# Kernel optimization log

Hardware: AMD Instinct MI355X
Metric: run time of the kernel (lower is better)

The kernel has to match this reference:

```python
import jax, jax.numpy as jnp
import numpy as np

B, N, K, D, H, T = 32, 4096, 8, 256, 4, 3
DH = D // H
SCALE = DH ** -0.5
EPS = 1e-8
HID = 256


def layernorm(x, w, b, eps=1e-5):
    m = jnp.mean(x, axis=-1, keepdims=True)
    v = jnp.var(x, axis=-1, keepdims=True)
    return (x - m) * jax.lax.rsqrt(v + eps) * w + b


def setup_inputs() -> dict:
    key = jax.random.key(0)
    ks = jax.random.split(key, 20)
    p = 0.02
    inp = {
        "x": jax.random.normal(ks[0], (B, N, D), jnp.float32),
        "noise": jax.random.normal(ks[1], (B, K, D), jnp.float32),
        "mu": jax.random.normal(ks[2], (1, 1, D), jnp.float32),
        "log_sigma": jax.random.normal(ks[3], (1, 1, D), jnp.float32) * p,
        "norm_in_w": jnp.ones((D,), jnp.float32), "norm_in_b": jnp.zeros((D,), jnp.float32),
        "norm_slot_w": jnp.ones((D,), jnp.float32), "norm_slot_b": jnp.zeros((D,), jnp.float32),
        "norm_mlp_w": jnp.ones((D,), jnp.float32), "norm_mlp_b": jnp.zeros((D,), jnp.float32),
        "Wq": jax.random.normal(ks[4], (D, D), jnp.float32) * p,
        "Wk": jax.random.normal(ks[5], (D, D), jnp.float32) * p,
        "Wv": jax.random.normal(ks[6], (D, D), jnp.float32) * p,
        "Wo": jax.random.normal(ks[7], (D, D), jnp.float32) * p,
        "gru_Wih": jax.random.normal(ks[8], (3 * D, D), jnp.float32) * p,
        "gru_Whh": jax.random.normal(ks[9], (3 * D, D), jnp.float32) * p,
        "gru_bih": jnp.zeros((3 * D,), jnp.float32),
        "gru_bhh": jnp.zeros((3 * D,), jnp.float32),
        "mlp_W1": jax.random.normal(ks[10], (HID, D), jnp.float32) * p,
        "mlp_b1": jnp.zeros((HID,), jnp.float32),
        "mlp_W2": jax.random.normal(ks[11], (D, HID), jnp.float32) * p,
        "mlp_b2": jnp.zeros((D,), jnp.float32),
    }
    return inp


def _split(t):
    # [b, n, D] -> [b, H, n, d_h]
    b, n, _ = t.shape
    return t.reshape(b, n, H, DH).transpose(0, 2, 1, 3)


def _merge(t):
    # [b, H, n, d_h] -> [b, n, D]
    b, h, n, d = t.shape
    return t.transpose(0, 2, 1, 3).reshape(b, n, h * d)


def _step(slots, k_feat, v_feat, p):
    b, k, d = slots.shape
    q = _split(layernorm(slots, p["norm_slot_w"], p["norm_slot_b"]) @ p["Wq"].T)
    dots = jnp.einsum("bhkd,bhnd->bhkn", q, k_feat) * SCALE
    attn = jax.nn.softmax(dots, axis=2)              # softmax over slot (query) axis
    attn = attn / (jnp.sum(attn, axis=-1, keepdims=True) + EPS)  # renorm over keys
    upd = _merge(jnp.einsum("bhkn,bhnd->bhkd", attn, v_feat)) @ p["Wo"].T
    # GRUCell(update, slots)
    gi = upd @ p["gru_Wih"].T + p["gru_bih"]
    gh = slots @ p["gru_Whh"].T + p["gru_bhh"]
    i_r, i_z, i_n = jnp.split(gi, 3, axis=-1)
    h_r, h_z, h_n = jnp.split(gh, 3, axis=-1)
    r = jax.nn.sigmoid(i_r + h_r)
    z = jax.nn.sigmoid(i_z + h_z)
    n = jnp.tanh(i_n + r * h_n)
    slots = (1.0 - z) * n + z * slots
    h1 = jax.nn.relu(layernorm(slots, p["norm_mlp_w"], p["norm_mlp_b"]) @ p["mlp_W1"].T + p["mlp_b1"])
    return slots + h1 @ p["mlp_W2"].T + p["mlp_b2"]


def reference(x, noise, mu, log_sigma, norm_in_w, norm_in_b, norm_slot_w, norm_slot_b,
              norm_mlp_w, norm_mlp_b, Wq, Wk, Wv, Wo, gru_Wih, gru_Whh, gru_bih, gru_bhh,
              mlp_W1, mlp_b1, mlp_W2, mlp_b2):
    p = dict(norm_slot_w=norm_slot_w, norm_slot_b=norm_slot_b, norm_mlp_w=norm_mlp_w,
             norm_mlp_b=norm_mlp_b, Wq=Wq, Wo=Wo, gru_Wih=gru_Wih, gru_Whh=gru_Whh,
             gru_bih=gru_bih, gru_bhh=gru_bhh, mlp_W1=mlp_W1, mlp_b1=mlp_b1,
             mlp_W2=mlp_W2, mlp_b2=mlp_b2)
    slots = mu + jnp.exp(log_sigma) * noise          # [B, K, D]
    xn = layernorm(x, norm_in_w, norm_in_b)
    k_feat = _split(xn @ Wk.T)                       # [B, H, N, d_h]
    v_feat = _split(xn @ Wv.T)
    for _ in range(T):
        slots = _step(slots, k_feat, v_feat, p)
    return slots
```

## Files before the change

### kernel.cpp

```cpp
#include <hip/hip_runtime.h>
#include <stdint.h>

typedef unsigned short ushort_t;
typedef __attribute__((ext_vector_type(8))) short bfrag;
typedef __attribute__((ext_vector_type(4))) float ffrag;

#define B_  32
#define K_  8
#define N_  4096
#define D_  256
#define H_  4
#define DH_ 64

__device__ __forceinline__ ushort_t f2bf(float f) {
  unsigned int u = __builtin_bit_cast(unsigned int, f);
  u += 0x7FFFu + ((u >> 16) & 1u);
  return (ushort_t)(u >> 16);
}

__global__ __launch_bounds__(256) void k_stats(const float* __restrict__ x,
                                               float2* __restrict__ stats) {
  int row = blockIdx.x * 4 + (threadIdx.x >> 6);
  int lane = threadIdx.x & 63;
  const float4* xr = (const float4*)(x + (size_t)row * 256);
  float4 v = xr[lane];
  float s = v.x + v.y + v.z + v.w;
  float q = v.x*v.x + v.y*v.y + v.z*v.z + v.w*v.w;
  #pragma unroll
  for (int off = 32; off >= 1; off >>= 1) { s += __shfl_xor(s, off); q += __shfl_xor(q, off); }
  if (lane == 0) {
    float m = s * (1.f/256.f);
    float var = q * (1.f/256.f) - m * m;
    stats[row] = make_float2(m, rsqrtf(var + 1e-5f));
  }
}

__global__ __launch_bounds__(256) void k_prep_wkv(const float* __restrict__ Wk, const float* __restrict__ Wv,
                                                  const float* __restrict__ lnw, const float* __restrict__ lnb,
                                                  ushort_t* __restrict__ wkv,
                                                  float* __restrict__ c1, float* __restrict__ c2) {
  int n = blockIdx.x;
  int i = threadIdx.x;
  float wv = (n < 256) ? Wk[n*256 + i] : Wv[(n-256)*256 + i];
  float wp = lnw[i] * wv;
  wkv[n*256 + i] = f2bf(wp);
  float p1 = wp, p2 = lnb[i] * wv;
  #pragma unroll
  for (int off = 32; off >= 1; off >>= 1) { p1 += __shfl_xor(p1, off); p2 += __shfl_xor(p2, off); }
  __shared__ float r1[4], r2[4];
  int w = threadIdx.x >> 6;
  if ((threadIdx.x & 63) == 0) { r1[w] = p1; r2[w] = p2; }
  __syncthreads();
  if (threadIdx.x == 0) { c1[n] = r1[0]+r1[1]+r1[2]+r1[3]; c2[n] = r2[0]+r2[1]+r2[2]+r2[3]; }
}

__global__ __launch_bounds__(256) void k_prep_wf(const float* __restrict__ Wih, const float* __restrict__ Wo,
                                                 float* __restrict__ Wf) {
  int j = blockIdx.x;
  int i = threadIdx.x;
  __shared__ float row[256];
  row[i] = Wih[j*256 + i];
  __syncthreads();
  float acc = 0.f;
  #pragma unroll 8
  for (int t = 0; t < 256; ++t) acc += row[t] * Wo[t*256 + i];
  Wf[j*256 + i] = acc;
}

__device__ __forceinline__ void row_ln_256(float (*S)[256], float (*L)[256],
                                           const float* __restrict__ w, const float* __restrict__ b, int t) {
  int k = t >> 5, ln = t & 31;
  float s = 0.f, q = 0.f;
  #pragma unroll
  for (int j = 0; j < 8; ++j) { float v = S[k][ln + j*32]; s += v; q += v*v; }
  #pragma unroll
  for (int off = 16; off >= 1; off >>= 1) { s += __shfl_xor(s, off); q += __shfl_xor(q, off); }
  float m = s * (1.f/256.f);
  float rstd = rsqrtf(q * (1.f/256.f) - m*m + 1e-5f);
  #pragma unroll
  for (int j = 0; j < 8; ++j) {
    int c = ln + j*32;
    L[k][c] = (S[k][c] - m) * rstd * w[c] + b[c];
  }
}

__device__ __forceinline__ void qproj(float (*L)[256], const float* __restrict__ Wq,
                                      ushort_t* __restrict__ qbuf, int b, int t) {
  int c = t;
  const float4* Wrow = (const float4*)(Wq + (size_t)c * 256);
  float acc[8];
  #pragma unroll
  for (int k = 0; k < 8; ++k) acc[k] = 0.f;
  for (int i = 0; i < 64; ++i) {
    float4 wv = Wrow[i];
    #pragma unroll
    for (int k = 0; k < 8; ++k) {
      float4 xv = *((const float4*)&L[k][0] + i);
      acc[k] = fmaf(xv.x, wv.x, fmaf(xv.y, wv.y, fmaf(xv.z, wv.z, fmaf(xv.w, wv.w, acc[k]))));
    }
  }
  int h = c >> 6, dh = c & 63;
  ushort_t* dst = qbuf + ((size_t)(b*4 + h) * 16) * 64 + dh;
  #pragma unroll
  for (int k = 0; k < 8; ++k) dst[k*64] = f2bf(acc[k] * 0.125f);
  #pragma unroll
  for (int k = 8; k < 16; ++k) dst[k*64] = 0;
}

__global__ __launch_bounds__(256) void k_init(const float* __restrict__ noise, const float* __restrict__ mu,
                                              const float* __restrict__ lsig, float* __restrict__ slots,
                                              const float* __restrict__ nsw, const float* __restrict__ nsb,
                                              const float* __restrict__ Wq, ushort_t* __restrict__ qbuf) {
  int b = blockIdx.x, t = threadIdx.x;
  __shared__ float S[8][256];
  __shared__ float L[8][256];
  float e = __expf(lsig[t]);
  float m = mu[t];
  #pragma unroll
  for (int k = 0; k < 8; ++k) {
    float v = m + e * noise[((size_t)(b*8+k))*256 + t];
    S[k][t] = v;
    slots[((size_t)(b*8+k))*256 + t] = v;
  }
  __syncthreads();
  row_ln_256(S, L, nsw, nsb, t);
  __syncthreads();
  qproj(L, Wq, qbuf, b, t);
}

__global__ __launch_bounds__(256, 2) void k_gemm(const float* __restrict__ x, const float2* __restrict__ stats,
                                                 const ushort_t* __restrict__ wkv,
                                                 const float* __restrict__ c1, const float* __restrict__ c2,
                                                 ushort_t* __restrict__ kf, ushort_t* __restrict__ vfT) {
  int mb = blockIdx.x, cb = blockIdx.y;
  int t = threadIdx.x;
  int w = t >> 6, l = t & 63;
  __shared__ uint4 ldsv[4096];
  char* lds = (char*)ldsv;
  const int m0 = mb * 128;
  const int col0 = cb * 128;

  int r0 = t >> 1, half = t & 1;
  float4 xa[8];
  uint4 wb[4];

  auto loadA = [&](int s) {
    const float4* src = (const float4*)(x + (size_t)(m0 + r0) * 256 + s*64 + half*32);
    #pragma unroll
    for (int i = 0; i < 8; ++i) xa[i] = src[i];
  };
  auto loadB = [&](int s) {
    const uint4* src = (const uint4*)(wkv + (size_t)(col0 + r0) * 256 + s*64 + half*32);
    #pragma unroll
    for (int i = 0; i < 4; ++i) wb[i] = src[i];
  };
  auto writeA = [&](char* Ab) {
    #pragma unroll
    for (int i = 0; i < 4; ++i) {
      float4 a = xa[2*i], b2 = xa[2*i+1];
      union { ushort_t us[8]; uint4 v; } u;
      u.us[0]=f2bf(a.x);  u.us[1]=f2bf(a.y);  u.us[2]=f2bf(a.z);  u.us[3]=f2bf(a.w);
      u.us[4]=f2bf(b2.x); u.us[5]=f2bf(b2.y); u.us[6]=f2bf(b2.z); u.us[7]=f2bf(b2.w);
      int byte = (r0*128 + half*64 + i*16) ^ ((r0 & 7) << 4);
      *(uint4*)(Ab + byte) = u.v;
    }
  };
  auto writeB = [&](char* Bb) {
    #pragma unroll
    for (int i = 0; i < 4; ++i) {
      int byte = (r0*128 + half*64 + i*16) ^ ((r0 & 7) << 4);
      *(uint4*)(Bb + byte) = wb[i];
    }
  };

  ffrag acc[4][4];
  #pragma unroll
  for (int i = 0; i < 4; ++i)
    #pragma unroll
    for (int j = 0; j < 4; ++j) acc[i][j] = (ffrag){0.f,0.f,0.f,0.f};

  int wm = w & 1, wn = w >> 1;
  int lrow = l & 15, lk = (l >> 4) * 8;

  loadA(0); loadB(0);
  writeA(lds + 0); writeB(lds + 32768);
  __syncthreads();

  for (int s = 0; s < 4; ++s) {
    char* Ac = lds + ((s & 1) ? 16384 : 0);
    char* Bc = lds + 32768 + ((s & 1) ? 16384 : 0);
    if (s < 3) { loadA(s+1); loadB(s+1); }
    #pragma unroll
    for (int kk = 0; kk < 2; ++kk) {
      bfrag af[4], bf[4];
      #pragma unroll
      for (int i = 0; i < 4; ++i) {
        int row = wm*64 + i*16 + lrow;
        int byte = (row*128 + (kk*32 + lk)*2) ^ ((row & 7) << 4);
        af[i] = *(const bfrag*)(Ac + byte);
      }
      #pragma unroll
      for (int j = 0; j < 4; ++j) {
        int row = wn*64 + j*16 + lrow;
        int byte = (row*128 + (kk*32 + lk)*2) ^ ((row & 7) << 4);
        bf[j] = *(const bfrag*)(Bc + byte);
      }
      #pragma unroll
      for (int i = 0; i < 4; ++i)
        #pragma unroll
        for (int j = 0; j < 4; ++j)
          acc[i][j] = __builtin_amdgcn_mfma_f32_16x16x32_bf16(af[i], bf[j], acc[i][j], 0, 0, 0);
    }
    if (s < 3) {
      char* An = lds + ((s & 1) ? 0 : 16384);
      char* Bn = lds + 32768 + ((s & 1) ? 0 : 16384);
      writeA(An); writeB(Bn);
    }
    __syncthreads();
  }

  int g = l >> 4, nl = l & 15;
  int b = m0 >> 12;
  int nx0 = m0 & 4095;
  if (cb < 2) {
    char* Ct = lds;
    #pragma unroll
    for (int i = 0; i < 4; ++i) {
      #pragma unroll
      for (int j = 0; j < 4; ++j) {
        int coll = wn*64 + j*16 + nl;
        float cc1 = c1[col0 + coll], cc2 = c2[col0 + coll];
        #pragma unroll
        for (int r = 0; r < 4; ++r) {
          int ml = wm*64 + i*16 + g*4 + r;
          float2 st = stats[m0 + ml];
          float val = st.y * (acc[i][j][r] - st.x * cc1) + cc2;
          *(ushort_t*)(Ct + (ml*136 + coll)*2) = f2bf(val);
        }
      }
    }
    __syncthreads();
    int m = t >> 1, hh = t & 1;
    int h = cb*2 + hh;
    ushort_t* dst = kf + ((size_t)((b*4 + h)*4096 + nx0 + m)) * 64;
    const char* srcr = Ct + m*272 + hh*128;
    #pragma unroll
    for (int jj = 0; jj < 8; ++jj)
      ((uint4*)dst)[jj] = *(const uint4*)(srcr + jj*16);
  } else {
    char* Ct = lds;
    #pragma unroll
    for (int i = 0; i < 4; ++i) {
      int mlbase = wm*64 + i*16 + g*4;
      #pragma unroll
      for (int j = 0; j < 4; ++j) {
        int coll = wn*64 + j*16 + nl;
        float cc1 = c1[col0 + coll], cc2 = c2[col0 + coll];
        ushort_t us[4];
        #pragma unroll
        for (int r = 0; r < 4; ++r) {
          float2 st = stats[m0 + mlbase + r];
          us[r] = f2bf(st.y * (acc[i][j][r] - st.x * cc1) + cc2);
        }
        uint2 pk = make_uint2((unsigned)us[0] | ((unsigned)us[1] << 16),
                              (unsigned)us[2] | ((unsigned)us[3] << 16));
        *(uint2*)(Ct + coll*272 + mlbase*2) = pk;
      }
    }
    __syncthreads();
    int colt = t >> 1, hh = t & 1;
    int h = (cb - 2)*2 + (colt >> 6);
    int dh = colt & 63;
    ushort_t* dst = vfT + ((size_t)((b*4 + h)*64 + dh)) * 4096 + nx0 + hh*64;
    const char* srcr = Ct + colt*272 + hh*128;
    #pragma unroll
    for (int jj = 0; jj < 8; ++jj)
      ((uint4*)dst)[jj] = *(const uint4*)(srcr + jj*16);
  }
}

__global__ __launch_bounds__(256, 2) void k_attn(const ushort_t* __restrict__ q, const ushort_t* __restrict__ kf,
                                                 const ushort_t* __restrict__ vfT,
                                                 float* __restrict__ updp, float* __restrict__ asump) {
  int split = blockIdx.x;
  int bh = blockIdx.y;
  int n0 = split * 256;
  int t = threadIdx.x, w = t >> 6, l = t & 63;
  __shared__ uint4 ldsv[4736];
  char* lds = (char*)ldsv;
  char* Kt = lds;
  char* Vt = lds + 32768;
  char* Pl = lds + 65536;
  char* Ql = lds + 73728;

  {
    const uint4* src = (const uint4*)(kf + ((size_t)bh*4096 + n0 + t) * 64);
    #pragma unroll
    for (int i = 0; i < 8; ++i) {
      int byte = (t*128 + i*16) ^ ((t & 7) << 4);
      *(uint4*)(Kt + byte) = src[i];
    }
  }
  {
    int d = t >> 2, seg = t & 3;
    const uint4* src = (const uint4*)(vfT + ((size_t)bh*64 + d) * 4096 + n0 + seg*64);
    #pragma unroll
    for (int i = 0; i < 4; ++i) {
      int byte = (d*512 + seg*128 + i*16) ^ ((d & 7) << 4);
      *(uint4*)(Vt + byte) = src[i];
    }
  }
  if (t < 128) {
    int k = t >> 3, seg = t & 7;
    uint4 v = *(const uint4*)(q + ((size_t)bh*16 + k) * 64 + seg*8);
    int byte = (k*128 + seg*16) ^ ((k & 7) << 4);
    *(uint4*)(Ql + byte) = v;
  }
  *(uint4*)(Pl + 4096 + t*16) = make_uint4(0,0,0,0);
  __syncthreads();

  int g = l >> 4, nl = l & 15, lk = g * 8;

  ffrag dacc[4];
  #pragma unroll
  for (int nt = 0; nt < 4; ++nt) {
    dacc[nt] = (ffrag){0.f,0.f,0.f,0.f};
    #pragma unroll
    for (int kk = 0; kk < 2; ++kk) {
      int qbyte = (nl*128 + (kk*32 + lk)*2) ^ ((nl & 7) << 4);
      bfrag af = *(const bfrag*)(Ql + qbyte);
      int row = w*64 + nt*16 + nl;
      int kbyte = (row*128 + (kk*32 + lk)*2) ^ ((row & 7) << 4);
      bfrag bf = *(const bfrag*)(Kt + kbyte);
      dacc[nt] = __builtin_amdgcn_mfma_f32_16x16x32_bf16(af, bf, dacc[nt], 0, 0, 0);
    }
  }

  float asr0 = 0.f, asr1 = 0.f, asr2 = 0.f, asr3 = 0.f;
  #pragma unroll
  for (int nt = 0; nt < 4; ++nt) {
    float d0 = dacc[nt][0], d1 = dacc[nt][1], d2 = dacc[nt][2], d3 = dacc[nt][3];
    float mx = fmaxf(fmaxf(d0, d1), fmaxf(d2, d3));
    mx = fmaxf(mx, __shfl_xor(mx, 16));
    float p0 = __expf(d0 - mx), p1 = __expf(d1 - mx), p2 = __expf(d2 - mx), p3 = __expf(d3 - mx);
    float sden = p0 + p1 + p2 + p3;
    sden += __shfl_xor(sden, 16);
    float inv = 1.f / sden;
    p0 *= inv; p1 *= inv; p2 *= inv; p3 *= inv;
    if (g < 2) {
      asr0 += p0; asr1 += p1; asr2 += p2; asr3 += p3;
      int n = w*64 + nt*16 + nl;
      int k0 = g*4;
      *(ushort_t*)(Pl + (((k0+0)*512 + n*2) ^ (((k0+0)&7) << 4))) = f2bf(p0);
      *(ushort_t*)(Pl + (((k0+1)*512 + n*2) ^ (((k0+1)&7) << 4))) = f2bf(p1);
      *(ushort_t*)(Pl + (((k0+2)*512 + n*2) ^ (((k0+2)&7) << 4))) = f2bf(p2);
      *(ushort_t*)(Pl + (((k0+3)*512 + n*2) ^ (((k0+3)&7) << 4))) = f2bf(p3);
    }
  }
  #pragma unroll
  for (int off = 8; off >= 1; off >>= 1) {
    asr0 += __shfl_xor(asr0, off); asr1 += __shfl_xor(asr1, off);
    asr2 += __shfl_xor(asr2, off); asr3 += __shfl_xor(asr3, off);
  }
  if (g < 2 && nl == 0) {
    float* dst = asump + (((size_t)bh*16 + split)*4 + w)*8 + g*4;
    dst[0] = asr0; dst[1] = asr1; dst[2] = asr2; dst[3] = asr3;
  }
  __syncthreads();

  ffrag pacc = (ffrag){0.f,0.f,0.f,0.f};
  #pragma unroll
  for (int ni = 0; ni < 8; ++ni) {
    int nn = ni * 32;
    int pbyte = (nl*512 + (nn + lk)*2) ^ ((nl & 7) << 4);
    bfrag af = *(const bfrag*)(Pl + pbyte);
    int d = w*16 + nl;
    int vbyte = (d*512 + (nn + lk)*2) ^ ((d & 7) << 4);
    bfrag bf = *(const bfrag*)(Vt + vbyte);
    pacc = __builtin_amdgcn_mfma_f32_16x16x32_bf16(af, bf, pacc, 0, 0, 0);
  }
  if (g < 2) {
    float* dst = updp + (((size_t)bh*16 + split)*8 + g*4)*64 + w*16 + nl;
    #pragma unroll
    for (int r = 0; r < 4; ++r) dst[r*64] = pacc[r];
  }
}

__global__ __launch_bounds__(256) void k_fin(const float* __restrict__ updp, const float* __restrict__ asump,
                                             float* __restrict__ upd) {
  int bh = blockIdx.x, t = threadIdx.x;
  __shared__ float asum[8];
  if (t < 8) {
    float a = 0.f;
    for (int s = 0; s < 64; ++s) a += asump[((size_t)bh*64 + s)*8 + t];
    asum[t] = a + 1e-8f;
  }
  __syncthreads();
  int b = bh >> 2, h = bh & 3;
  #pragma unroll
  for (int o = t; o < 512; o += 256) {
    int k = o >> 6, d = o & 63;
    float u = 0.f;
    for (int s = 0; s < 16; ++s) u += updp[(((size_t)bh*16 + s)*8 + k)*64 + d];
    upd[((size_t)(b*8 + k))*256 + h*64 + d] = u / asum[k];
  }
}

__global__ __launch_bounds__(256) void k_u1(const float* __restrict__ upd, const float* __restrict__ slots,
                                            const float* __restrict__ Wf, const float* __restrict__ Whh,
                                            const float* __restrict__ bih, const float* __restrict__ bhh,
                                            float* __restrict__ gi, float* __restrict__ gh) {
  int cb = blockIdx.x, b = blockIdx.y, t = threadIdx.x;
  int c = cb * 256 + t;
  bool isGi = (c < 768);
  __shared__ float X[8][256];
  const float* src = isGi ? upd : slots;
  #pragma unroll
  for (int k = 0; k < 8; ++k) X[k][t] = src[((size_t)(b*8+k))*256 + t];
  __syncthreads();
  int cc = isGi ? c : (c - 768);
  const float* Wrow = (isGi ? Wf : Whh) + (size_t)cc * 256;
  float bias = isGi ? bih[cc] : bhh[cc];
  float acc[8];
  #pragma unroll
  for (int k = 0; k < 8; ++k) acc[k] = bias;
  for (int i = 0; i < 64; ++i) {
    float4 wv = ((const float4*)Wrow)[i];
    #pragma unroll
    for (int k = 0; k < 8; ++k) {
      float4 xv = *((const float4*)&X[k][0] + i);
      acc[k] = fmaf(xv.x, wv.x, fmaf(xv.y, wv.y, fmaf(xv.z, wv.z, fmaf(xv.w, wv.w, acc[k]))));
    }
  }
  float* dst = isGi ? gi : gh;
  #pragma unroll
  for (int k = 0; k < 8; ++k) dst[((size_t)(b*8+k))*768 + cc] = acc[k];
}

__global__ __launch_bounds__(256) void k_u2(const float* __restrict__ gi, const float* __restrict__ gh,
                                            const float* __restrict__ slots_in, float* __restrict__ slots_out,
                                            const float* __restrict__ nmw, const float* __restrict__ nmb,
                                            const float* __restrict__ W1, const float* __restrict__ b1,
                                            const float* __restrict__ W2, const float* __restrict__ b2,
                                            const float* __restrict__ nsw, const float* __restrict__ nsb,
                                            const float* __restrict__ Wq, ushort_t* __restrict__ qbuf, int do_q) {
  int b = blockIdx.x, t = threadIdx.x;
  __shared__ float S[8][256];
  __shared__ float L[8][256];
  __shared__ float H1[8][256];
  #pragma unroll
  for (int k = 0; k < 8; ++k) {
    size_t gb = ((size_t)(b*8+k))*768;
    float ir = gi[gb + t],       hr = gh[gb + t];
    float iz = gi[gb + 256 + t], hz = gh[gb + 256 + t];
    float in_ = gi[gb + 512 + t], hn = gh[gb + 512 + t];
    float r = 1.f / (1.f + __expf(-(ir + hr)));
    float z = 1.f / (1.f + __expf(-(iz + hz)));
    float a = in_ + r * hn;
    float e2 = __expf(-2.f * fabsf(a));
    float nn = (1.f - e2) / (1.f + e2);
    nn = copysignf(nn, a);
    S[k][t] = (1.f - z) * nn + z * slots_in[((size_t)(b*8+k))*256 + t];
  }
  __syncthreads();
  row_ln_256(S, L, nmw, nmb, t);
  __syncthreads();
  {
    const float4* Wrow = (const float4*)(W1 + (size_t)t * 256);
    float bb = b1[t];
    float acc[8];
    #pragma unroll
    for (int k = 0; k < 8; ++k) acc[k] = bb;
    for (int i = 0; i < 64; ++i) {
      float4 wv = Wrow[i];
      #pragma unroll
      for (int k = 0; k < 8; ++k) {
        float4 xv = *((const float4*)&L[k][0] + i);
        acc[k] = fmaf(xv.x, wv.x, fmaf(xv.y, wv.y, fmaf(xv.z, wv.z, fmaf(xv.w, wv.w, acc[k]))));
      }
    }
    #pragma unroll
    for (int k = 0; k < 8; ++k) H1[k][t] = fmaxf(acc[k], 0.f);
  }
  __syncthreads();
  {
    const float4* Wrow = (const float4*)(W2 + (size_t)t * 256);
    float bb = b2[t];
    float acc[8];
    #pragma unroll
    for (int k = 0; k < 8; ++k) acc[k] = bb;
    for (int i = 0; i < 64; ++i) {
      float4 wv = Wrow[i];
      #pragma unroll
      for (int k = 0; k < 8; ++k) {
        float4 xv = *((const float4*)&H1[k][0] + i);
        acc[k] = fmaf(xv.x, wv.x, fmaf(xv.y, wv.y, fmaf(xv.z, wv.z, fmaf(xv.w, wv.w, acc[k]))));
      }
    }
    #pragma unroll
    for (int k = 0; k < 8; ++k) {
      float o = S[k][t] + acc[k];
      slots_out[((size_t)(b*8+k))*256 + t] = o;
      S[k][t] = o;
    }
  }
  __syncthreads();
  if (do_q) {
    row_ln_256(S, L, nsw, nsb, t);
    __syncthreads();
    qproj(L, Wq, qbuf, b, t);
  }
}

extern "C" void kernel_launch(void* const* d_in, const int* in_sizes, int n_in,
                              void* d_out, int out_size, void* d_ws, size_t ws_size,
                              hipStream_t stream) {
  (void)in_sizes; (void)n_in; (void)out_size; (void)ws_size;
  const float* x     = (const float*)d_in[0];
  const float* noise = (const float*)d_in[1];
  const float* mu    = (const float*)d_in[2];
  const float* lsig  = (const float*)d_in[3];
  const float* ninw  = (const float*)d_in[4];
  const float* ninb  = (const float*)d_in[5];
  const float* nsw   = (const float*)d_in[6];
  const float* nsb   = (const float*)d_in[7];
  const float* nmw   = (const float*)d_in[8];
  const float* nmb   = (const float*)d_in[9];
  const float* Wq    = (const float*)d_in[10];
  const float* Wk    = (const float*)d_in[11];
  const float* Wv    = (const float*)d_in[12];
  const float* Wo    = (const float*)d_in[13];
  const float* Wih   = (const float*)d_in[14];
  const float* Whh   = (const float*)d_in[15];
  const float* bih   = (const float*)d_in[16];
  const float* bhh   = (const float*)d_in[17];
  const float* W1    = (const float*)d_in[18];
  const float* b1    = (const float*)d_in[19];
  const float* W2    = (const float*)d_in[20];
  const float* b2    = (const float*)d_in[21];

  char* ws = (char*)d_ws;
  float2*   stats = (float2*)  (ws + 0);
  ushort_t* wkv   = (ushort_t*)(ws + 1048576);
  float*    c1    = (float*)   (ws + 1310720);
  float*    c2    = (float*)   (ws + 1312768);
  float*    Wf    = (float*)   (ws + 1314816);
  float*    slots = (float*)   (ws + 2101248);
  ushort_t* qbuf  = (ushort_t*)(ws + 2363392);
  float*    upd   = (float*)   (ws + 2625536);
  float*    gi    = (float*)   (ws + 2887680);
  float*    gh    = (float*)   (ws + 3674112);
  float*    asump = (float*)   (ws + 4460544);
  float*    updp  = (float*)   (ws + 4722688);
  ushort_t* kf    = (ushort_t*)(ws + 8916992);
  ushort_t* vfT   = (ushort_t*)(ws + 76025856);

  k_stats   <<<32768, 256, 0, stream>>>(x, stats);
  k_prep_wkv<<<512,   256, 0, stream>>>(Wk, Wv, ninw, ninb, wkv, c1, c2);
  k_prep_wf <<<768,   256, 0, stream>>>(Wih, Wo, Wf);
  k_init    <<<32,    256, 0, stream>>>(noise, mu, lsig, slots, nsw, nsb, Wq, qbuf);
  k_gemm    <<<dim3(1024, 4), 256, 0, stream>>>(x, stats, wkv, c1, c2, kf, vfT);

  float* outp = (float*)d_out;
  for (int it = 0; it < 3; ++it) {
    k_attn<<<dim3(16, 128), 256, 0, stream>>>(qbuf, kf, vfT, updp, asump);
    k_fin <<<128, 256, 0, stream>>>(updp, asump, upd);
    k_u1  <<<dim3(6, 32), 256, 0, stream>>>(upd, slots, Wf, Whh, bih, bhh, gi, gh);
    k_u2  <<<32, 256, 0, stream>>>(gi, gh, slots, (it == 2) ? outp : slots,
                                   nmw, nmb, W1, b1, W2, b2, nsw, nsb, Wq, qbuf, (it < 2) ? 1 : 0);
  }
}
```

Baseline: 644.1 us.

## Fuse layernorm stats into K/V GEMM, shrink LDS, read K/V directly in attention

The separate row-statistics kernel is removed. Mean and rstd are now accumulated in the GEMM's A-tile load path and shared through LDS, which avoids one extra full pass over x. The GEMM uses a smaller K-step with half the LDS, raises occupancy to 4 blocks per unit, and remaps block IDs into groups of 8. Its epilogue is split into two halves. The attention kernel drops its K/V LDS staging and reads MFMA fragments straight from global memory, and k_u2 is split across two blocks per batch; each of these trades memory locality or redundant weight reads for more parallelism.

```diff
diff --git a/kernel.cpp b/kernel.cpp
--- a/kernel.cpp
+++ b/kernel.cpp
@@ -16,23 +16,6 @@
   unsigned int u = __builtin_bit_cast(unsigned int, f);
   u += 0x7FFFu + ((u >> 16) & 1u);
   return (ushort_t)(u >> 16);
-}
-
-__global__ __launch_bounds__(256) void k_stats(const float* __restrict__ x,
-                                               float2* __restrict__ stats) {
-  int row = blockIdx.x * 4 + (threadIdx.x >> 6);
-  int lane = threadIdx.x & 63;
-  const float4* xr = (const float4*)(x + (size_t)row * 256);
-  float4 v = xr[lane];
-  float s = v.x + v.y + v.z + v.w;
-  float q = v.x*v.x + v.y*v.y + v.z*v.z + v.w*v.w;
-  #pragma unroll
-  for (int off = 32; off >= 1; off >>= 1) { s += __shfl_xor(s, off); q += __shfl_xor(q, off); }
-  if (lane == 0) {
-    float m = s * (1.f/256.f);
-    float var = q * (1.f/256.f) - m * m;
-    stats[row] = make_float2(m, rsqrtf(var + 1e-5f));
-  }
 }
 
 __global__ __launch_bounds__(256) void k_prep_wkv(const float* __restrict__ Wk, const float* __restrict__ Wv,
@@ -107,6 +90,46 @@
   for (int k = 8; k < 16; ++k) dst[k*64] = 0;
 }
 
+__device__ __forceinline__ void row_ln_4x(float (*S)[256], float (*L)[256],
+                                          const float* __restrict__ w, const float* __restrict__ b, int t) {
+  int k = t >> 6, ln = t & 63;
+  float s = 0.f, q = 0.f;
+  #pragma unroll
+  for (int j = 0; j < 4; ++j) { float v = S[k][ln + j*64]; s += v; q += v*v; }
+  #pragma unroll
+  for (int off = 32; off >= 1; off >>= 1) { s += __shfl_xor(s, off); q += __shfl_xor(q, off); }
+  float m = s * (1.f/256.f);
+  float rstd = rsqrtf(q * (1.f/256.f) - m*m + 1e-5f);
+  #pragma unroll
+  for (int j = 0; j < 4; ++j) {
+    int c = ln + j*64;
+    L[k][c] = (S[k][c] - m) * rstd * w[c] + b[c];
+  }
+}
+
+__device__ __forceinline__ void qproj4(float (*L)[256], const float* __restrict__ Wq,
+                                       ushort_t* __restrict__ qbuf, int b, int ks0, int t) {
+  int c = t;
+  const float4* Wrow = (const float4*)(Wq + (size_t)c * 256);
+  float acc[4];
+  #pragma unroll
+  for (int k = 0; k < 4; ++k) acc[k] = 0.f;
+  for (int i = 0; i < 64; ++i) {
+    float4 wv = Wrow[i];
+    #pragma unroll
+    for (int k = 0; k < 4; ++k) {
+      float4 xv = *((const float4*)&L[k][0] + i);
+      acc[k] = fmaf(xv.x, wv.x, fmaf(xv.y, wv.y, fmaf(xv.z, wv.z, fmaf(xv.w, wv.w, acc[k]))));
+    }
+  }
+  int h = c >> 6, dh = c & 63;
+  ushort_t* dst = qbuf + ((size_t)(b*4 + h) * 16) * 64 + dh;
+  #pragma unroll
+  for (int k = 0; k < 4; ++k) dst[(ks0 + k)*64] = f2bf(acc[k] * 0.125f);
+  #pragma unroll
+  for (int k = 0; k < 4; ++k) dst[(8 + ks0 + k)*64] = 0;
+}
+
 __global__ __launch_bounds__(256) void k_init(const float* __restrict__ noise, const float* __restrict__ mu,
                                               const float* __restrict__ lsig, float* __restrict__ slots,
                                               const float* __restrict__ nsw, const float* __restrict__ nsb,
@@ -128,210 +151,205 @@
   qproj(L, Wq, qbuf, b, t);
 }
 
-__global__ __launch_bounds__(256, 2) void k_gemm(const float* __restrict__ x, const float2* __restrict__ stats,
+__global__ __launch_bounds__(256, 4) void k_gemm(const float* __restrict__ x,
                                                  const ushort_t* __restrict__ wkv,
                                                  const float* __restrict__ c1, const float* __restrict__ c2,
                                                  ushort_t* __restrict__ kf, ushort_t* __restrict__ vfT) {
-  int mb = blockIdx.x, cb = blockIdx.y;
-  int t = threadIdx.x;
-  int w = t >> 6, l = t & 63;
-  __shared__ uint4 ldsv[4096];
+  int bid = blockIdx.x;
+  int wg = (bid & 7) * 512 + (bid >> 3);
+  int mb = wg >> 2, cb = wg & 3;
+  int t = threadIdx.x, w = t >> 6, l = t & 63;
+  __shared__ uint4 ldsv[2048];
   char* lds = (char*)ldsv;
-  const int m0 = mb * 128;
-  const int col0 = cb * 128;
-
+  const int m0 = mb * 128, col0 = cb * 128;
   int r0 = t >> 1, half = t & 1;
-  float4 xa[8];
-  uint4 wb[4];
+
+  float4 xa[4];
+  uint4 wb[2];
+  float ssum = 0.f, sqsum = 0.f;
+  int swzW = ((r0 >> 1) & 3) << 4;
 
   auto loadA = [&](int s) {
-    const float4* src = (const float4*)(x + (size_t)(m0 + r0) * 256 + s*64 + half*32);
-    #pragma unroll
-    for (int i = 0; i < 8; ++i) xa[i] = src[i];
+    const float4* src = (const float4*)(x + (size_t)(m0 + r0) * 256 + s*32 + half*16);
+    #pragma unroll
+    for (int i = 0; i < 4; ++i) xa[i] = src[i];
   };
   auto loadB = [&](int s) {
-    const uint4* src = (const uint4*)(wkv + (size_t)(col0 + r0) * 256 + s*64 + half*32);
-    #pragma unroll
-    for (int i = 0; i < 4; ++i) wb[i] = src[i];
+    const uint4* src = (const uint4*)(wkv + (size_t)(col0 + r0) * 256 + s*32 + half*16);
+    wb[0] = src[0]; wb[1] = src[1];
   };
   auto writeA = [&](char* Ab) {
     #pragma unroll
-    for (int i = 0; i < 4; ++i) {
+    for (int i = 0; i < 2; ++i) {
       float4 a = xa[2*i], b2 = xa[2*i+1];
+      ssum  += a.x + a.y + a.z + a.w + b2.x + b2.y + b2.z + b2.w;
+      sqsum += a.x*a.x + a.y*a.y + a.z*a.z + a.w*a.w
+             + b2.x*b2.x + b2.y*b2.y + b2.z*b2.z + b2.w*b2.w;
       union { ushort_t us[8]; uint4 v; } u;
       u.us[0]=f2bf(a.x);  u.us[1]=f2bf(a.y);  u.us[2]=f2bf(a.z);  u.us[3]=f2bf(a.w);
       u.us[4]=f2bf(b2.x); u.us[5]=f2bf(b2.y); u.us[6]=f2bf(b2.z); u.us[7]=f2bf(b2.w);
-      int byte = (r0*128 + half*64 + i*16) ^ ((r0 & 7) << 4);
-      *(uint4*)(Ab + byte) = u.v;
+      *(uint4*)(Ab + r0*64 + ((half*32 + i*16) ^ swzW)) = u.v;
     }
   };
   auto writeB = [&](char* Bb) {
     #pragma unroll
+    for (int i = 0; i < 2; ++i)
+      *(uint4*)(Bb + r0*64 + ((half*32 + i*16) ^ swzW)) = wb[i];
+  };
+
+  ffrag acc[4][4];
+  #pragma unroll
+  for (int i = 0; i < 4; ++i)
+    #pragma unroll
+    for (int j = 0; j < 4; ++j) acc[i][j] = (ffrag){0.f,0.f,0.f,0.f};
+
+  int wm = w & 1, wn = w >> 1;
+  int lrow = l & 15, lkb = ((l >> 4) * 8) * 2;
+
+  loadA(0); loadB(0);
+  writeA(lds); writeB(lds + 16384);
+  __syncthreads();
+
+  for (int s = 0; s < 8; ++s) {
+    char* Ac = lds + ((s & 1) << 13);
+    char* Bc = lds + 16384 + ((s & 1) << 13);
+    if (s < 7) { loadA(s+1); loadB(s+1); }
+    bfrag bfr[4];
+    #pragma unroll
+    for (int j = 0; j < 4; ++j) {
+      int row = wn*64 + j*16 + lrow;
+      bfr[j] = *(const bfrag*)(Bc + row*64 + (lkb ^ (((row >> 1) & 3) << 4)));
+    }
+    #pragma unroll
     for (int i = 0; i < 4; ++i) {
-      int byte = (r0*128 + half*64 + i*16) ^ ((r0 & 7) << 4);
-      *(uint4*)(Bb + byte) = wb[i];
-    }
-  };
-
-  ffrag acc[4][4];
-  #pragma unroll
-  for (int i = 0; i < 4; ++i)
-    #pragma unroll
-    for (int j = 0; j < 4; ++j) acc[i][j] = (ffrag){0.f,0.f,0.f,0.f};
-
-  int wm = w & 1, wn = w >> 1;
-  int lrow = l & 15, lk = (l >> 4) * 8;
-
-  loadA(0); loadB(0);
-  writeA(lds + 0); writeB(lds + 32768);
-  __syncthreads();
-
-  for (int s = 0; s < 4; ++s) {
-    char* Ac = lds + ((s & 1) ? 16384 : 0);
-    char* Bc = lds + 32768 + ((s & 1) ? 16384 : 0);
-    if (s < 3) { loadA(s+1); loadB(s+1); }
-    #pragma unroll
-    for (int kk = 0; kk < 2; ++kk) {
-      bfrag af[4], bf[4];
+      int row = wm*64 + i*16 + lrow;
+      bfrag afr = *(const bfrag*)(Ac + row*64 + (lkb ^ (((row >> 1) & 3) << 4)));
       #pragma unroll
-      for (int i = 0; i < 4; ++i) {
-        int row = wm*64 + i*16 + lrow;
-        int byte = (row*128 + (kk*32 + lk)*2) ^ ((row & 7) << 4);
-        af[i] = *(const bfrag*)(Ac + byte);
-      }
-      #pragma unroll
-      for (int j = 0; j < 4; ++j) {
-        int row = wn*64 + j*16 + lrow;
-        int byte = (row*128 + (kk*32 + lk)*2) ^ ((row & 7) << 4);
-        bf[j] = *(const bfrag*)(Bc + byte);
-      }
-      #pragma unroll
-      for (int i = 0; i < 4; ++i)
+      for (int j = 0; j < 4; ++j)
+        acc[i][j] = __builtin_amdgcn_mfma_f32_16x16x32_bf16(afr, bfr[j], acc[i][j], 0, 0, 0);
+    }
+    if (s < 7) {
+      char* An = lds + (((s+1) & 1) << 13);
+      char* Bn = lds + 16384 + (((s+1) & 1) << 13);
+      writeA(An); writeB(Bn);
+    }
+    __syncthreads();
+  }
+
+  float s2 = ssum  + __shfl_xor(ssum, 1);
+  float q2 = sqsum + __shfl_xor(sqsum, 1);
+  float* statm = (float*)(lds + 28672);
+  float* statr = (float*)(lds + 29184);
+  if (half == 0) {
+    float mm = s2 * (1.f/256.f);
+    statm[r0] = mm;
+    statr[r0] = rsqrtf(q2 * (1.f/256.f) - mm*mm + 1e-5f);
+  }
+  __syncthreads();
+
+  int g = l >> 4, nl = l & 15;
+  int b = m0 >> 12, nx0 = m0 & 4095;
+  if (cb < 2) {
+    for (int p = 0; p < 2; ++p) {
+      if (wm == p) {
         #pragma unroll
-        for (int j = 0; j < 4; ++j)
-          acc[i][j] = __builtin_amdgcn_mfma_f32_16x16x32_bf16(af[i], bf[j], acc[i][j], 0, 0, 0);
-    }
-    if (s < 3) {
-      char* An = lds + ((s & 1) ? 0 : 16384);
-      char* Bn = lds + 32768 + ((s & 1) ? 0 : 16384);
-      writeA(An); writeB(Bn);
-    }
-    __syncthreads();
-  }
-
-  int g = l >> 4, nl = l & 15;
-  int b = m0 >> 12;
-  int nx0 = m0 & 4095;
-  if (cb < 2) {
-    char* Ct = lds;
-    #pragma unroll
-    for (int i = 0; i < 4; ++i) {
-      #pragma unroll
-      for (int j = 0; j < 4; ++j) {
-        int coll = wn*64 + j*16 + nl;
-        float cc1 = c1[col0 + coll], cc2 = c2[col0 + coll];
-        #pragma unroll
-        for (int r = 0; r < 4; ++r) {
-          int ml = wm*64 + i*16 + g*4 + r;
-          float2 st = stats[m0 + ml];
-          float val = st.y * (acc[i][j][r] - st.x * cc1) + cc2;
-          *(ushort_t*)(Ct + (ml*136 + coll)*2) = f2bf(val);
+        for (int i = 0; i < 4; ++i) {
+          #pragma unroll
+          for (int j = 0; j < 4; ++j) {
+            int coll = wn*64 + j*16 + nl;
+            float cc1 = c1[col0 + coll], cc2 = c2[col0 + coll];
+            #pragma unroll
+            for (int r = 0; r < 4; ++r) {
+              int ml = i*16 + g*4 + r;
+              int mlg = p*64 + ml;
+              float val = statr[mlg] * (acc[i][j][r] - statm[mlg] * cc1) + cc2;
+              *(ushort_t*)(lds + (ml*136 + coll)*2) = f2bf(val);
+            }
+          }
         }
       }
-    }
-    __syncthreads();
-    int m = t >> 1, hh = t & 1;
-    int h = cb*2 + hh;
-    ushort_t* dst = kf + ((size_t)((b*4 + h)*4096 + nx0 + m)) * 64;
-    const char* srcr = Ct + m*272 + hh*128;
-    #pragma unroll
-    for (int jj = 0; jj < 8; ++jj)
-      ((uint4*)dst)[jj] = *(const uint4*)(srcr + jj*16);
+      __syncthreads();
+      {
+        int mloc = t >> 2, hh = (t >> 1) & 1, qq = t & 1;
+        int h = cb*2 + hh;
+        ushort_t* dst = kf + ((size_t)((b*4 + h)*4096 + nx0 + p*64 + mloc)) * 64 + qq*32;
+        const char* srcr = lds + mloc*272 + hh*128 + qq*64;
+        #pragma unroll
+        for (int jj = 0; jj < 4; ++jj)
+          ((uint4*)dst)[jj] = *(const uint4*)(srcr + jj*16);
+      }
+      __syncthreads();
+    }
   } else {
-    char* Ct = lds;
-    #pragma unroll
-    for (int i = 0; i < 4; ++i) {
-      int mlbase = wm*64 + i*16 + g*4;
-      #pragma unroll
-      for (int j = 0; j < 4; ++j) {
-        int coll = wn*64 + j*16 + nl;
-        float cc1 = c1[col0 + coll], cc2 = c2[col0 + coll];
-        ushort_t us[4];
+    for (int p = 0; p < 2; ++p) {
+      if (wn == p) {
         #pragma unroll
-        for (int r = 0; r < 4; ++r) {
-          float2 st = stats[m0 + mlbase + r];
-          us[r] = f2bf(st.y * (acc[i][j][r] - st.x * cc1) + cc2);
+        for (int i = 0; i < 4; ++i) {
+          int mlb = wm*64 + i*16 + g*4;
+          #pragma unroll
+          for (int j = 0; j < 4; ++j) {
+            int coll = j*16 + nl;
+            int collg = p*64 + coll;
+            float cc1 = c1[col0 + collg], cc2 = c2[col0 + collg];
+            ushort_t us[4];
+            #pragma unroll
+            for (int r = 0; r < 4; ++r)
+              us[r] = f2bf(statr[mlb+r] * (acc[i][j][r] - statm[mlb+r] * cc1) + cc2);
+            *(uint2*)(lds + coll*272 + mlb*2) =
+              make_uint2((unsigned)us[0] | ((unsigned)us[1] << 16),
+                         (unsigned)us[2] | ((unsigned)us[3] << 16));
+          }
         }
-        uint2 pk = make_uint2((unsigned)us[0] | ((unsigned)us[1] << 16),
-                              (unsigned)us[2] | ((unsigned)us[3] << 16));
-        *(uint2*)(Ct + coll*272 + mlbase*2) = pk;
       }
-    }
-    __syncthreads();
-    int colt = t >> 1, hh = t & 1;
-    int h = (cb - 2)*2 + (colt >> 6);
-    int dh = colt & 63;
-    ushort_t* dst = vfT + ((size_t)((b*4 + h)*64 + dh)) * 4096 + nx0 + hh*64;
-    const char* srcr = Ct + colt*272 + hh*128;
-    #pragma unroll
-    for (int jj = 0; jj < 8; ++jj)
-      ((uint4*)dst)[jj] = *(const uint4*)(srcr + jj*16);
-  }
-}
-
-__global__ __launch_bounds__(256, 2) void k_attn(const ushort_t* __restrict__ q, const ushort_t* __restrict__ kf,
+      __syncthreads();
+      {
+        int cl = t >> 2, seg = t & 3;
+        int collg = p*64 + cl;
+        int h = (cb - 2)*2 + (collg >> 6);
+        int dh = collg & 63;
+        ushort_t* dst = vfT + ((size_t)((b*4 + h)*64 + dh)) * 4096 + nx0 + seg*32;
+        const char* srcr = lds + cl*272 + seg*64;
+        #pragma unroll
+        for (int jj = 0; jj < 4; ++jj)
+          ((uint4*)dst)[jj] = *(const uint4*)(srcr + jj*16);
+      }
+      __syncthreads();
+    }
+  }
+}
+
+__global__ __launch_bounds__(256, 4) void k_attn(const ushort_t* __restrict__ q, const ushort_t* __restrict__ kf,
                                                  const ushort_t* __restrict__ vfT,
                                                  float* __restrict__ updp, float* __restrict__ asump) {
   int split = blockIdx.x;
   int bh = blockIdx.y;
   int n0 = split * 256;
   int t = threadIdx.x, w = t >> 6, l = t & 63;
-  __shared__ uint4 ldsv[4736];
+  __shared__ uint4 ldsv[640];
   char* lds = (char*)ldsv;
-  char* Kt = lds;
-  char* Vt = lds + 32768;
-  char* Pl = lds + 65536;
-  char* Ql = lds + 73728;
-
-  {
-    const uint4* src = (const uint4*)(kf + ((size_t)bh*4096 + n0 + t) * 64);
-    #pragma unroll
-    for (int i = 0; i < 8; ++i) {
-      int byte = (t*128 + i*16) ^ ((t & 7) << 4);
-      *(uint4*)(Kt + byte) = src[i];
-    }
-  }
-  {
-    int d = t >> 2, seg = t & 3;
-    const uint4* src = (const uint4*)(vfT + ((size_t)bh*64 + d) * 4096 + n0 + seg*64);
-    #pragma unroll
-    for (int i = 0; i < 4; ++i) {
-      int byte = (d*512 + seg*128 + i*16) ^ ((d & 7) << 4);
-      *(uint4*)(Vt + byte) = src[i];
-    }
-  }
+  char* Pl = lds;
+  char* Ql = lds + 8192;
+
   if (t < 128) {
     int k = t >> 3, seg = t & 7;
     uint4 v = *(const uint4*)(q + ((size_t)bh*16 + k) * 64 + seg*8);
-    int byte = (k*128 + seg*16) ^ ((k & 7) << 4);
-    *(uint4*)(Ql + byte) = v;
+    *(uint4*)(Ql + k*128 + ((seg*16) ^ ((k & 7) << 4))) = v;
   }
   *(uint4*)(Pl + 4096 + t*16) = make_uint4(0,0,0,0);
   __syncthreads();
 
   int g = l >> 4, nl = l & 15, lk = g * 8;
+  const ushort_t* kbase = kf + ((size_t)bh*4096 + n0) * 64;
 
   ffrag dacc[4];
   #pragma unroll
   for (int nt = 0; nt < 4; ++nt) {
     dacc[nt] = (ffrag){0.f,0.f,0.f,0.f};
+    int row = w*64 + nt*16 + nl;
     #pragma unroll
     for (int kk = 0; kk < 2; ++kk) {
-      int qbyte = (nl*128 + (kk*32 + lk)*2) ^ ((nl & 7) << 4);
-      bfrag af = *(const bfrag*)(Ql + qbyte);
-      int row = w*64 + nt*16 + nl;
-      int kbyte = (row*128 + (kk*32 + lk)*2) ^ ((row & 7) << 4);
-      bfrag bf = *(const bfrag*)(Kt + kbyte);
+      bfrag af = *(const bfrag*)(Ql + nl*128 + (((kk*32 + lk)*2) ^ ((nl & 7) << 4)));
+      bfrag bf = *(const bfrag*)(kbase + (size_t)row*64 + kk*32 + lk);
       dacc[nt] = __builtin_amdgcn_mfma_f32_16x16x32_bf16(af, bf, dacc[nt], 0, 0, 0);
     }
   }
@@ -368,15 +386,14 @@
   }
   __syncthreads();
 
+  const ushort_t* vbase = vfT + ((size_t)bh*64) * 4096 + n0;
   ffrag pacc = (ffrag){0.f,0.f,0.f,0.f};
+  int d = w*16 + nl;
   #pragma unroll
   for (int ni = 0; ni < 8; ++ni) {
     int nn = ni * 32;
-    int pbyte = (nl*512 + (nn + lk)*2) ^ ((nl & 7) << 4);
-    bfrag af = *(const bfrag*)(Pl + pbyte);
-    int d = w*16 + nl;
-    int vbyte = (d*512 + (nn + lk)*2) ^ ((d & 7) << 4);
-    bfrag bf = *(const bfrag*)(Vt + vbyte);
+    bfrag af = *(const bfrag*)(Pl + nl*512 + (((nn + lk)*2) ^ ((nl & 7) << 4)));
+    bfrag bf = *(const bfrag*)(vbase + (size_t)d*4096 + nn + lk);
     pacc = __builtin_amdgcn_mfma_f32_16x16x32_bf16(af, bf, pacc, 0, 0, 0);
   }
   if (g < 2) {
@@ -444,15 +461,18 @@
                                             const float* __restrict__ W2, const float* __restrict__ b2,
                                             const float* __restrict__ nsw, const float* __restrict__ nsb,
                                             const float* __restrict__ Wq, ushort_t* __restrict__ qbuf, int do_q) {
-  int b = blockIdx.x, t = threadIdx.x;
-  __shared__ float S[8][256];
-  __shared__ float L[8][256];
-  __shared__ float H1[8][256];
-  #pragma unroll
-  for (int k = 0; k < 8; ++k) {
-    size_t gb = ((size_t)(b*8+k))*768;
-    float ir = gi[gb + t],       hr = gh[gb + t];
-    float iz = gi[gb + 256 + t], hz = gh[gb + 256 + t];
+  int bid = blockIdx.x;
+  int b = bid >> 1, ks0 = (bid & 1) * 4;
+  int t = threadIdx.x;
+  __shared__ float S[4][256];
+  __shared__ float L[4][256];
+  __shared__ float H1[4][256];
+  #pragma unroll
+  for (int k = 0; k < 4; ++k) {
+    int slot = b*8 + ks0 + k;
+    size_t gb = (size_t)slot * 768;
+    float ir = gi[gb + t],        hr = gh[gb + t];
+    float iz = gi[gb + 256 + t],  hz = gh[gb + 256 + t];
     float in_ = gi[gb + 512 + t], hn = gh[gb + 512 + t];
     float r = 1.f / (1.f + __expf(-(ir + hr)));
     float z = 1.f / (1.f + __expf(-(iz + hz)));
@@ -460,55 +480,56 @@
     float e2 = __expf(-2.f * fabsf(a));
     float nn = (1.f - e2) / (1.f + e2);
     nn = copysignf(nn, a);
-    S[k][t] = (1.f - z) * nn + z * slots_in[((size_t)(b*8+k))*256 + t];
-  }
-  __syncthreads();
-  row_ln_256(S, L, nmw, nmb, t);
+    S[k][t] = (1.f - z) * nn + z * slots_in[(size_t)slot * 256 + t];
+  }
+  __syncthreads();
+  row_ln_4x(S, L, nmw, nmb, t);
   __syncthreads();
   {
     const float4* Wrow = (const float4*)(W1 + (size_t)t * 256);
     float bb = b1[t];
-    float acc[8];
-    #pragma unroll
-    for (int k = 0; k < 8; ++k) acc[k] = bb;
+    float acc[4];
+    #pragma unroll
+    for (int k = 0; k < 4; ++k) acc[k] = bb;
     for (int i = 0; i < 64; ++i) {
       float4 wv = Wrow[i];
       #pragma unroll
-      for (int k = 0; k < 8; ++k) {
+      for (int k = 0; k < 4; ++k) {
         float4 xv = *((const float4*)&L[k][0] + i);
         acc[k] = fmaf(xv.x, wv.x, fmaf(xv.y, wv.y, fmaf(xv.z, wv.z, fmaf(xv.w, wv.w, acc[k]))));
       }
     }
     #pragma unroll
-    for (int k = 0; k < 8; ++k) H1[k][t] = fmaxf(acc[k], 0.f);
+    for (int k = 0; k < 4; ++k) H1[k][t] = fmaxf(acc[k], 0.f);
   }
   __syncthreads();
   {
     const float4* Wrow = (const float4*)(W2 + (size_t)t * 256);
     float bb = b2[t];
-    float acc[8];
-    #pragma unroll
-    for (int k = 0; k < 8; ++k) acc[k] = bb;
+    float acc[4];
+    #pragma unroll
+    for (int k = 0; k < 4; ++k) acc[k] = bb;
     for (int i = 0; i < 64; ++i) {
       float4 wv = Wrow[i];
       #pragma unroll
-      for (int k = 0; k < 8; ++k) {
+      for (int k = 0; k < 4; ++k) {
         float4 xv = *((const float4*)&H1[k][0] + i);
         acc[k] = fmaf(xv.x, wv.x, fmaf(xv.y, wv.y, fmaf(xv.z, wv.z, fmaf(xv.w, wv.w, acc[k]))));
       }
     }
     #pragma unroll
-    for (int k = 0; k < 8; ++k) {
+    for (int k = 0; k < 4; ++k) {
+      int slot = b*8 + ks0 + k;
       float o = S[k][t] + acc[k];
-      slots_out[((size_t)(b*8+k))*256 + t] = o;
+      slots_out[(size_t)slot * 256 + t] = o;
       S[k][t] = o;
     }
   }
   __syncthreads();
   if (do_q) {
-    row_ln_256(S, L, nsw, nsb, t);
+    row_ln_4x(S, L, nsw, nsb, t);
     __syncthreads();
-    qproj(L, Wq, qbuf, b, t);
+    qproj4(L, Wq, qbuf, b, ks0, t);
   }
 }
 
@@ -540,33 +561,31 @@
   const float* b2    = (const float*)d_in[21];
 
   char* ws = (char*)d_ws;
-  float2*   stats = (float2*)  (ws + 0);
-  ushort_t* wkv   = (ushort_t*)(ws + 1048576);
-  float*    c1    = (float*)   (ws + 1310720);
-  float*    c2    = (float*)   (ws + 1312768);
-  float*    Wf    = (float*)   (ws + 1314816);
-  float*    slots = (float*)   (ws + 2101248);
-  ushort_t* qbuf  = (ushort_t*)(ws + 2363392);
-  float*    upd   = (float*)   (ws + 2625536);
-  float*    gi    = (float*)   (ws + 2887680);
-  float*    gh    = (float*)   (ws + 3674112);
-  float*    asump = (float*)   (ws + 4460544);
-  float*    updp  = (float*)   (ws + 4722688);
-  ushort_t* kf    = (ushort_t*)(ws + 8916992);
-  ushort_t* vfT   = (ushort_t*)(ws + 76025856);
-
-  k_stats   <<<32768, 256, 0, stream>>>(x, stats);
-  k_prep_wkv<<<512,   256, 0, stream>>>(Wk, Wv, ninw, ninb, wkv, c1, c2);
-  k_prep_wf <<<768,   256, 0, stream>>>(Wih, Wo, Wf);
-  k_init    <<<32,    256, 0, stream>>>(noise, mu, lsig, slots, nsw, nsb, Wq, qbuf);
-  k_gemm    <<<dim3(1024, 4), 256, 0, stream>>>(x, stats, wkv, c1, c2, kf, vfT);
+  ushort_t* wkv   = (ushort_t*)(ws + 0);
+  float*    c1    = (float*)   (ws + 262144);
+  float*    c2    = (float*)   (ws + 264192);
+  float*    Wf    = (float*)   (ws + 266240);
+  float*    slots = (float*)   (ws + 1052672);
+  ushort_t* qbuf  = (ushort_t*)(ws + 1314816);
+  float*    upd   = (float*)   (ws + 1576960);
+  float*    gi    = (float*)   (ws + 1839104);
+  float*    gh    = (float*)   (ws + 2625536);
+  float*    asump = (float*)   (ws + 3411968);
+  float*    updp  = (float*)   (ws + 3674112);
+  ushort_t* kf    = (ushort_t*)(ws + 7868416);
+  ushort_t* vfT   = (ushort_t*)(ws + 74977280);
+
+  k_prep_wkv<<<512,  256, 0, stream>>>(Wk, Wv, ninw, ninb, wkv, c1, c2);
+  k_gemm    <<<4096, 256, 0, stream>>>(x, wkv, c1, c2, kf, vfT);
+  k_prep_wf <<<768,  256, 0, stream>>>(Wih, Wo, Wf);
+  k_init    <<<32,   256, 0, stream>>>(noise, mu, lsig, slots, nsw, nsb, Wq, qbuf);
 
   float* outp = (float*)d_out;
   for (int it = 0; it < 3; ++it) {
     k_attn<<<dim3(16, 128), 256, 0, stream>>>(qbuf, kf, vfT, updp, asump);
     k_fin <<<128, 256, 0, stream>>>(updp, asump, upd);
     k_u1  <<<dim3(6, 32), 256, 0, stream>>>(upd, slots, Wf, Whh, bih, bhh, gi, gh);
-    k_u2  <<<32, 256, 0, stream>>>(gi, gh, slots, (it == 2) ? outp : slots,
+    k_u2  <<<64, 256, 0, stream>>>(gi, gh, slots, (it == 2) ? outp : slots,
                                    nmw, nmb, W1, b1, W2, b2, nsw, nsb, Wq, qbuf, (it < 2) ? 1 : 0);
   }
 }
```

Result: slower. 982.4 us (+52.5%).
